# Performance work log

Measured on AMD Instinct MI355X. Metric: run time of the kernel, lower is better.

The kernel has to match this reference:

```python
import jax, jax.numpy as jnp
import numpy as np

HIDDEN = 256
N_HEADS = 4
HEAD_DIM = HIDDEN // N_HEADS
SCALE = float(np.sqrt(HEAD_DIM))


def setup_inputs() -> dict:
    key = jax.random.key(0)
    ks = jax.random.split(key, 10)
    B, NQ, NKV = 2, 4096, 4096
    s = 1.0 / np.sqrt(HIDDEN)
    inp = {
        "query": jax.random.normal(ks[0], (B, NQ, HIDDEN), dtype=jnp.float32),
        "key_value": jax.random.normal(ks[1], (B, NKV, HIDDEN), dtype=jnp.float32),
        "kv_mask": jnp.ones((B, NKV), dtype=jnp.int32),
        "Wq": jax.random.uniform(ks[2], (HIDDEN, HIDDEN), jnp.float32, -s, s),
        "bq": jnp.zeros((HIDDEN,), jnp.float32),
        "Wk": jax.random.uniform(ks[3], (HIDDEN, HIDDEN), jnp.float32, -s, s),
        "bk": jnp.zeros((HIDDEN,), jnp.float32),
        "Wv": jax.random.uniform(ks[4], (HIDDEN, HIDDEN), jnp.float32, -s, s),
        "bv": jnp.zeros((HIDDEN,), jnp.float32),
        "Wo": jax.random.uniform(ks[5], (HIDDEN, HIDDEN), jnp.float32, -s, s),
        "bo": jnp.zeros((HIDDEN,), jnp.float32),
    }
    return inp


def reference(query, key_value, kv_mask, Wq, bq, Wk, bk, Wv, bv, Wo, bo):
    B, NQ, D = query.shape
    NKV = key_value.shape[1]
    # projections; reshape to (B, H, S, Dh)
    q = (query @ Wq + bq).reshape(B, NQ, N_HEADS, HEAD_DIM).transpose(0, 2, 1, 3)
    k = (key_value @ Wk + bk).reshape(B, NKV, N_HEADS, HEAD_DIM).transpose(0, 2, 1, 3)
    v = (key_value @ Wv + bv).reshape(B, NKV, N_HEADS, HEAD_DIM).transpose(0, 2, 1, 3)
    # scores: (B, H, NQ, NKV)
    attn = jnp.einsum("bhqd,bhkd->bhqk", q, k) / SCALE
    mask = (kv_mask != 0)[:, None, None, :]  # (B,1,1,NKV)
    attn = jnp.where(mask, attn, -jnp.inf)
    attn = jax.nn.softmax(attn, axis=-1)
    # dropout is identity in eval mode (reference is deterministic)
    out = jnp.einsum("bhqk,bhkd->bhqd", attn, v)
    out = out.transpose(0, 2, 1, 3).reshape(B, NQ, D)
    return out @ Wo + bo
```

## Files before the change

kernel.cpp:

```cpp
#include <hip/hip_runtime.h>
#include <hip/hip_bf16.h>
#include <math.h>

#define HID   256
#define NHEADS  4
#define HDIM   64
#define SEQ  4096
#define BATCH   2
#define MTOK (BATCH * SEQ)
#define LOG2E 1.44269504088896340736f
#define MFIX  8.0f

typedef short bf16x8 __attribute__((ext_vector_type(8)));
typedef float f32x4  __attribute__((ext_vector_type(4)));

__device__ __forceinline__ unsigned short f2b(float f) {
  union { float f; unsigned u; } v; v.f = f;
  return (unsigned short)((v.u + 0x7FFFu + ((v.u >> 16) & 1u)) >> 16);
}
__device__ __forceinline__ unsigned pkb(float a, float b) {
  __hip_bfloat162 h = __float22bfloat162_rn(make_float2(a, b));
  union { __hip_bfloat162 h; unsigned u; } v; v.h = h;
  return v.u;
}
__device__ __forceinline__ float exp2_(float x) {
#if __has_builtin(__builtin_amdgcn_exp2f)
  return __builtin_amdgcn_exp2f(x);
#else
  return exp2f(x);
#endif
}

__global__ __launch_bounds__(256)
void cast_wt(const float* __restrict__ W0, const float* __restrict__ W1,
             const float* __restrict__ W2, const float* __restrict__ W3,
             unsigned short* __restrict__ Wt) {
  __shared__ float t[64][65];
  const float* Ws[4] = {W0, W1, W2, W3};
  const float scl[4] = {0.125f * LOG2E, 1.f, 1.f, 1.f};
  const int wsel = blockIdx.y;
  const float* W = Ws[wsel];
  const float s = scl[wsel];
  unsigned short* O = Wt + (size_t)wsel * HID * HID;
  const int kt = (blockIdx.x & 3) * 64, nt = (blockIdx.x >> 2) * 64;
  const int tid = threadIdx.x;
#pragma unroll
  for (int p = 0; p < 4; ++p) {
    int i = p * 256 + tid;
    int r = i >> 4, c4 = (i & 15) * 4;
    *(float4*)&t[r][c4] = *(const float4*)&W[(size_t)(kt + r) * HID + nt + c4];
  }
  __syncthreads();
#pragma unroll
  for (int p = 0; p < 4; ++p) {
    int i = p * 256 + tid;
    int rn = i >> 4, ck = (i & 15) * 4;
    ushort4 o;
    o.x = f2b(t[ck + 0][rn] * s);
    o.y = f2b(t[ck + 1][rn] * s);
    o.z = f2b(t[ck + 2][rn] * s);
    o.w = f2b(t[ck + 3][rn] * s);
    *(ushort4*)&O[(size_t)(nt + rn) * HID + kt + ck] = o;
  }
}

__global__ __launch_bounds__(256)
void gemm_qkv(const float* __restrict__ query, const float* __restrict__ keyv,
              const unsigned short* __restrict__ wts,
              const float* __restrict__ bq, const float* __restrict__ bk,
              const float* __restrict__ bv,
              unsigned short* qp, unsigned short* kp, unsigned short* vtp) {
  __shared__ __align__(16) unsigned short As[2][64][136];
  __shared__ __align__(16) unsigned short Bs[64][136];
  float (*L)[68] = (float (*)[68])&Bs[0][0];

  const int tid = threadIdx.x;
  const int w = tid >> 6, lane = tid & 63, lq = lane & 15, quad = lane >> 4;
  const int wm = w & 1, wn = w >> 1;
  const int z = blockIdx.y;
  const int m0 = blockIdx.x * 64;

  const float* A = (z == 0) ? query : keyv;
  const unsigned short* Bt = wts + (size_t)z * HID * HID;
  const float* bias = (z == 0) ? bq : ((z == 1) ? bk : bv);
  const float bscale = (z == 0) ? 0.125f * LOG2E : 1.0f;

#pragma unroll
  for (int p = 0; p < 16; ++p) {
    int i = p * 256 + tid;
    int r = i >> 6, c4 = (i & 63) * 4;
    float4 f4 = *(const float4*)&A[(size_t)(m0 + r) * HID + c4];
    unsigned lo = pkb(f4.x, f4.y), hi = pkb(f4.z, f4.w);
    *(uint2*)&As[c4 >> 7][r][c4 & 127] = make_uint2(lo, hi);
  }
  __syncthreads();

  for (int n = 0; n < 4; ++n) {
    const int n0 = n * 64;
    f32x4 acc[2][2];
#pragma unroll
    for (int i = 0; i < 2; ++i)
#pragma unroll
      for (int j = 0; j < 2; ++j) acc[i][j] = (f32x4){0.f, 0.f, 0.f, 0.f};

#pragma unroll
    for (int kt = 0; kt < 2; ++kt) {
#pragma unroll
      for (int p = 0; p < 4; ++p) {
        int i = p * 256 + tid;
        int r = i >> 4, c8 = (i & 15) * 8;
        *(uint4*)&Bs[r][c8] =
            *(const uint4*)&Bt[(size_t)(n0 + r) * HID + kt * 128 + c8];
      }
      __syncthreads();
#pragma unroll
      for (int ks = 0; ks < 4; ++ks) {
        bf16x8 a0 = *(const bf16x8*)&As[kt][wm * 32 + lq][ks * 32 + quad * 8];
        bf16x8 a1 = *(const bf16x8*)&As[kt][wm * 32 + 16 + lq][ks * 32 + quad * 8];
        bf16x8 b0 = *(const bf16x8*)&Bs[wn * 32 + lq][ks * 32 + quad * 8];
        bf16x8 b1 = *(const bf16x8*)&Bs[wn * 32 + 16 + lq][ks * 32 + quad * 8];
        acc[0][0] = __builtin_amdgcn_mfma_f32_16x16x32_bf16(a0, b0, acc[0][0], 0, 0, 0);
        acc[0][1] = __builtin_amdgcn_mfma_f32_16x16x32_bf16(a0, b1, acc[0][1], 0, 0, 0);
        acc[1][0] = __builtin_amdgcn_mfma_f32_16x16x32_bf16(a1, b0, acc[1][0], 0, 0, 0);
        acc[1][1] = __builtin_amdgcn_mfma_f32_16x16x32_bf16(a1, b1, acc[1][1], 0, 0, 0);
      }
      __syncthreads();
    }

#pragma unroll
    for (int ni = 0; ni < 2; ++ni) {
      const float bv = bias[n0 + wn * 32 + ni * 16 + lq] * bscale;
#pragma unroll
      for (int mi = 0; mi < 2; ++mi)
#pragma unroll
        for (int r = 0; r < 4; ++r)
          L[wm * 32 + mi * 16 + quad * 4 + r][wn * 32 + ni * 16 + lq] =
              acc[mi][ni][r] + bv;
    }
    __syncthreads();

    if (z == 2) {
      const int nn = tid >> 2, mb4 = (tid & 3) * 16;
      __align__(16) unsigned short tmp[16];
#pragma unroll
      for (int j = 0; j < 16; ++j) {
        int p = mb4 + j;
        int k = ((p & 3) << 4) + (p >> 2);
        tmp[j] = f2b(L[k][nn]);
      }
      *(uint4*)&vtp[(size_t)(n0 + nn) * MTOK + m0 + mb4]     = *(uint4*)&tmp[0];
      *(uint4*)&vtp[(size_t)(n0 + nn) * MTOK + m0 + mb4 + 8] = *(uint4*)&tmp[8];
    } else {
      unsigned short* Y = (z == 0) ? qp : kp;
      const int r = tid >> 2, cb = (tid & 3) * 16;
      __align__(16) unsigned short tmp[16];
#pragma unroll
      for (int j = 0; j < 4; ++j) {
        float4 v4 = *(const float4*)&L[r][cb + j * 4];
        *(uint2*)&tmp[j * 4] = make_uint2(pkb(v4.x, v4.y), pkb(v4.z, v4.w));
      }
      *(uint4*)&Y[(size_t)(m0 + r) * HID + n0 + cb]     = *(uint4*)&tmp[0];
      *(uint4*)&Y[(size_t)(m0 + r) * HID + n0 + cb + 8] = *(uint4*)&tmp[8];
    }
    __syncthreads();
  }
}

__global__ __launch_bounds__(256)
void gemm_out(const unsigned short* __restrict__ ao,
              const unsigned short* __restrict__ wot,
              const float* __restrict__ bo, float* __restrict__ out) {
  __shared__ __align__(16) unsigned short As[64][136];
  __shared__ __align__(16) unsigned short Bs[64][136];
  float (*L)[68] = (float (*)[68])&As[0][0];

  const int tid = threadIdx.x;
  const int w = tid >> 6, lane = tid & 63, lq = lane & 15, quad = lane >> 4;
  const int wm = w & 1, wn = w >> 1;
  const int m0 = blockIdx.y * 64, n0 = blockIdx.x * 64;

  f32x4 acc[2][2];
#pragma unroll
  for (int i = 0; i < 2; ++i)
#pragma unroll
    for (int j = 0; j < 2; ++j) acc[i][j] = (f32x4){0.f, 0.f, 0.f, 0.f};

#pragma unroll
  for (int kt = 0; kt < 2; ++kt) {
    const int k0 = kt * 128;
#pragma unroll
    for (int p = 0; p < 4; ++p) {
      int i = p * 256 + tid;
      int r = i >> 4, c8 = (i & 15) * 8;
      *(uint4*)&As[r][c8] = *(const uint4*)&ao[(size_t)(m0 + r) * HID + k0 + c8];
      *(uint4*)&Bs[r][c8] = *(const uint4*)&wot[(size_t)(n0 + r) * HID + k0 + c8];
    }
    __syncthreads();
#pragma unroll
    for (int ks = 0; ks < 4; ++ks) {
      bf16x8 a0 = *(const bf16x8*)&As[wm * 32 + lq][ks * 32 + quad * 8];
      bf16x8 a1 = *(const bf16x8*)&As[wm * 32 + 16 + lq][ks * 32 + quad * 8];
      bf16x8 b0 = *(const bf16x8*)&Bs[wn * 32 + lq][ks * 32 + quad * 8];
      bf16x8 b1 = *(const bf16x8*)&Bs[wn * 32 + 16 + lq][ks * 32 + quad * 8];
      acc[0][0] = __builtin_amdgcn_mfma_f32_16x16x32_bf16(a0, b0, acc[0][0], 0, 0, 0);
      acc[0][1] = __builtin_amdgcn_mfma_f32_16x16x32_bf16(a0, b1, acc[0][1], 0, 0, 0);
      acc[1][0] = __builtin_amdgcn_mfma_f32_16x16x32_bf16(a1, b0, acc[1][0], 0, 0, 0);
      acc[1][1] = __builtin_amdgcn_mfma_f32_16x16x32_bf16(a1, b1, acc[1][1], 0, 0, 0);
    }
    __syncthreads();
  }

#pragma unroll
  for (int ni = 0; ni < 2; ++ni) {
    const float bv = bo[n0 + wn * 32 + ni * 16 + lq];
#pragma unroll
    for (int mi = 0; mi < 2; ++mi)
#pragma unroll
      for (int r = 0; r < 4; ++r)
        L[wm * 32 + mi * 16 + quad * 4 + r][wn * 32 + ni * 16 + lq] =
            acc[mi][ni][r] + bv;
  }
  __syncthreads();

  const int r = tid >> 2, cb = (tid & 3) * 16;
#pragma unroll
  for (int j = 0; j < 4; ++j) {
    float4 v4 = *(const float4*)&L[r][cb + j * 4];
    *(float4*)&out[(size_t)(m0 + r) * HID + n0 + cb + j * 4] = v4;
  }
}

__global__ __launch_bounds__(512, 1)
void flash_attn_mfma(const unsigned short* __restrict__ Qp,
                     const unsigned short* __restrict__ Kp,
                     const unsigned short* __restrict__ Vtp,
                     const int* __restrict__ mask,
                     unsigned short* __restrict__ Ao) {
  __shared__ __align__(16) unsigned short Ks[2][128][72];
  __shared__ __align__(16) unsigned short Vt[2][64][136];
  __shared__ __align__(16) unsigned short Ps[8][32][72];
  __shared__ float mb[2][128];

  float (*Ored)[32][68] = (float (*)[32][68])&Ps[0][0][0];
  float* Lred = (float*)((char*)&Ps[0][0][0] + sizeof(float) * 4 * 32 * 68);

  const int tid = threadIdx.x;
  const int w = tid >> 6, lane = tid & 63, lq = lane & 15, quad = lane >> 4;
  const int qg = w >> 1, kg = w & 1;
  const int bh = blockIdx.x;
  const int b = bh >> 2, h = bh & 3;
  const int q0 = blockIdx.y * 128;
  const int qbase = b * SEQ + q0, kvbase = b * SEQ, coff = h * HDIM;

  const int rk0 = tid >> 3,          ck0 = (tid & 7) * 8;
  const int rk1 = (512 + tid) >> 3,  ck1 = ((512 + tid) & 7) * 8;
  const int rv0 = tid >> 4,          cv0 = (tid & 15) * 8;
  const int rv1 = (512 + tid) >> 4,  cv1 = ((512 + tid) & 15) * 8;

  bf16x8 qf[2][2];
#pragma unroll
  for (int m = 0; m < 2; ++m) {
    const unsigned short* qr =
        &Qp[(size_t)(qbase + qg * 32 + m * 16 + lq) * HID + coff + quad * 8];
    qf[m][0] = *(const bf16x8*)&qr[0];
    qf[m][1] = *(const bf16x8*)&qr[32];
  }

  const short oneb = (short)0x3F80;
  const bf16x8 ones = {oneb, oneb, oneb, oneb, oneb, oneb, oneb, oneb};

  f32x4 o[2][4], ls2[2];
#pragma unroll
  for (int m = 0; m < 2; ++m) {
    ls2[m] = (f32x4){0.f, 0.f, 0.f, 0.f};
#pragma unroll
    for (int dc = 0; dc < 4; ++dc) o[m][dc] = (f32x4){0.f, 0.f, 0.f, 0.f};
  }

  {
    *(uint4*)&Ks[0][rk0][ck0] =
        *(const uint4*)&Kp[(size_t)(kvbase + rk0) * HID + coff + ck0];
    *(uint4*)&Ks[0][rk1][ck1] =
        *(const uint4*)&Kp[(size_t)(kvbase + rk1) * HID + coff + ck1];
    *(uint4*)&Vt[0][rv0][cv0] =
        *(const uint4*)&Vtp[(size_t)(coff + rv0) * MTOK + kvbase + cv0];
    *(uint4*)&Vt[0][rv1][cv1] =
        *(const uint4*)&Vtp[(size_t)(coff + rv1) * MTOK + kvbase + cv1];
    if (tid < 128) mb[0][tid] = mask[kvbase + tid] ? -MFIX : -1e30f;
  }
  __syncthreads();

  const int NT = SEQ / 128;
  for (int t = 0; t < NT; ++t) {
    const int cur = t & 1, nxt = cur ^ 1;
    const bool pf = (t + 1 < NT);

    uint4 kA, kB, vA, vB;
    float mbr = 0.f;
    if (pf) {
      const int k0n = (t + 1) * 128;
      kA = *(const uint4*)&Kp[(size_t)(kvbase + k0n + rk0) * HID + coff + ck0];
      kB = *(const uint4*)&Kp[(size_t)(kvbase + k0n + rk1) * HID + coff + ck1];
      vA = *(const uint4*)&Vtp[(size_t)(coff + rv0) * MTOK + kvbase + k0n + cv0];
      vB = *(const uint4*)&Vtp[(size_t)(coff + rv1) * MTOK + kvbase + k0n + cv1];
      if (tid < 128) mbr = mask[kvbase + k0n + tid] ? -MFIX : -1e30f;
    }

    f32x4 sc[2][4];
#pragma unroll
    for (int m = 0; m < 2; ++m)
#pragma unroll
      for (int c = 0; c < 4; ++c) sc[m][c] = (f32x4){0.f, 0.f, 0.f, 0.f};
#pragma unroll
    for (int c = 0; c < 4; ++c) {
      bf16x8 kb0 = *(const bf16x8*)&Ks[cur][kg * 64 + c * 16 + lq][quad * 8];
      bf16x8 kb1 = *(const bf16x8*)&Ks[cur][kg * 64 + c * 16 + lq][32 + quad * 8];
      sc[0][c] = __builtin_amdgcn_mfma_f32_16x16x32_bf16(qf[0][0], kb0, sc[0][c], 0, 0, 0);
      sc[0][c] = __builtin_amdgcn_mfma_f32_16x16x32_bf16(qf[0][1], kb1, sc[0][c], 0, 0, 0);
      sc[1][c] = __builtin_amdgcn_mfma_f32_16x16x32_bf16(qf[1][0], kb0, sc[1][c], 0, 0, 0);
      sc[1][c] = __builtin_amdgcn_mfma_f32_16x16x32_bf16(qf[1][1], kb1, sc[1][c], 0, 0, 0);
    }
    float mbias[4];
#pragma unroll
    for (int c = 0; c < 4; ++c) mbias[c] = mb[cur][kg * 64 + c * 16 + lq];

#pragma unroll
    for (int m = 0; m < 2; ++m) {
#pragma unroll
      for (int r = 0; r < 4; ++r) {
        const int row = m * 16 + quad * 4 + r;
        unsigned a0 = pkb(exp2_(sc[m][0][r] + mbias[0]),
                          exp2_(sc[m][1][r] + mbias[1]));
        unsigned a1 = pkb(exp2_(sc[m][2][r] + mbias[2]),
                          exp2_(sc[m][3][r] + mbias[3]));
        *(uint2*)&Ps[w][row][lq * 4] = make_uint2(a0, a1);
      }
    }

#pragma unroll
    for (int i = 0; i < 2; ++i) {
      bf16x8 pa0 = *(const bf16x8*)&Ps[w][lq][i * 32 + quad * 8];
      bf16x8 pa1 = *(const bf16x8*)&Ps[w][16 + lq][i * 32 + quad * 8];
      ls2[0] = __builtin_amdgcn_mfma_f32_16x16x32_bf16(pa0, ones, ls2[0], 0, 0, 0);
      ls2[1] = __builtin_amdgcn_mfma_f32_16x16x32_bf16(pa1, ones, ls2[1], 0, 0, 0);
#pragma unroll
      for (int dc = 0; dc < 4; ++dc) {
        bf16x8 vb =
            *(const bf16x8*)&Vt[cur][dc * 16 + lq][kg * 64 + i * 32 + quad * 8];
        o[0][dc] = __builtin_amdgcn_mfma_f32_16x16x32_bf16(pa0, vb, o[0][dc], 0, 0, 0);
        o[1][dc] = __builtin_amdgcn_mfma_f32_16x16x32_bf16(pa1, vb, o[1][dc], 0, 0, 0);
      }
    }

    if (pf) {
      *(uint4*)&Ks[nxt][rk0][ck0] = kA;
      *(uint4*)&Ks[nxt][rk1][ck1] = kB;
      *(uint4*)&Vt[nxt][rv0][cv0] = vA;
      *(uint4*)&Vt[nxt][rv1][cv1] = vB;
      if (tid < 128) mb[nxt][tid] = mbr;
    }
    __syncthreads();
  }

  if (kg == 1) {
#pragma unroll
    for (int m = 0; m < 2; ++m) {
#pragma unroll
      for (int r = 0; r < 4; ++r) {
        const int row = m * 16 + quad * 4 + r;
        if (lq == 0) Lred[qg * 32 + row] = ls2[m][r];
#pragma unroll
        for (int dc = 0; dc < 4; ++dc)
          Ored[qg][row][dc * 16 + lq] = o[m][dc][r];
      }
    }
  }
  __syncthreads();
  if (kg == 0) {
#pragma unroll
    for (int m = 0; m < 2; ++m) {
#pragma unroll
      for (int r = 0; r < 4; ++r) {
        const int row = m * 16 + quad * 4 + r;
        const float l = ls2[m][r] + Lred[qg * 32 + row];
        const float inv = 1.f / l;
        const size_t grow = (size_t)(qbase + qg * 32 + row);
#pragma unroll
        for (int dc = 0; dc < 4; ++dc) {
          const float val = (o[m][dc][r] + Ored[qg][row][dc * 16 + lq]) * inv;
          Ao[grow * HID + coff + dc * 16 + lq] = f2b(val);
        }
      }
    }
  }
}

extern "C" void kernel_launch(void* const* d_in, const int* in_sizes, int n_in,
                              void* d_out, int out_size, void* d_ws, size_t ws_size,
                              hipStream_t stream) {
  const float* query = (const float*)d_in[0];
  const float* keyv  = (const float*)d_in[1];
  const int*   mask  = (const int*)d_in[2];
  const float* Wq = (const float*)d_in[3];
  const float* bq = (const float*)d_in[4];
  const float* Wk = (const float*)d_in[5];
  const float* bk = (const float*)d_in[6];
  const float* Wv = (const float*)d_in[7];
  const float* bv = (const float*)d_in[8];
  const float* Wo = (const float*)d_in[9];
  const float* bo = (const float*)d_in[10];
  float* out = (float*)d_out;

  unsigned short* wts = (unsigned short*)d_ws;
  unsigned short* qp  = wts + (size_t)4 * HID * HID;
  unsigned short* kp  = qp  + (size_t)MTOK * HID;
  unsigned short* vtp = kp  + (size_t)MTOK * HID;
  unsigned short* ao  = vtp + (size_t)MTOK * HID;

  const unsigned short* wo_t = wts + 3 * HID * HID;

  dim3 blk(256);
  hipLaunchKernelGGL(cast_wt, dim3(16, 4), blk, 0, stream, Wq, Wk, Wv, Wo, wts);

  dim3 qkvgrid(MTOK / 64, 3);
  hipLaunchKernelGGL(gemm_qkv, qkvgrid, blk, 0, stream,
                     query, keyv, wts, bq, bk, bv, qp, kp, vtp);

  dim3 fgrid(BATCH * NHEADS, SEQ / 128);
  hipLaunchKernelGGL(flash_attn_mfma, fgrid, dim3(512), 0, stream,
                     qp, kp, vtp, mask, ao);

  dim3 ogrid(HID / 64, MTOK / 64);
  hipLaunchKernelGGL(gemm_out, ogrid, blk, 0, stream, ao, wo_t, bo, out);
}
```

Before: 159.5 us.

## Fuse weight transpose-cast into projection GEMMs and drop cast kernel

Removes the separate weight cast/transpose kernel. The QKV and output GEMMs now read fp32 weights directly, scale and convert them to bf16, and scatter them transposed into shared memory. The output GEMM is restructured so each block holds a 64-row A tile and loops over all four N tiles, matching the QKV kernel. This saves one kernel launch and a workspace round trip. In exchange, every block redoes the weight conversion with scalar 2-byte transposed LDS stores that may bank-conflict, and the output GEMM grid shrinks fourfold.

```diff
diff --git a/kernel.cpp b/kernel.cpp
--- a/kernel.cpp
+++ b/kernel.cpp
@@ -32,41 +32,9 @@
 }
 
 __global__ __launch_bounds__(256)
-void cast_wt(const float* __restrict__ W0, const float* __restrict__ W1,
-             const float* __restrict__ W2, const float* __restrict__ W3,
-             unsigned short* __restrict__ Wt) {
-  __shared__ float t[64][65];
-  const float* Ws[4] = {W0, W1, W2, W3};
-  const float scl[4] = {0.125f * LOG2E, 1.f, 1.f, 1.f};
-  const int wsel = blockIdx.y;
-  const float* W = Ws[wsel];
-  const float s = scl[wsel];
-  unsigned short* O = Wt + (size_t)wsel * HID * HID;
-  const int kt = (blockIdx.x & 3) * 64, nt = (blockIdx.x >> 2) * 64;
-  const int tid = threadIdx.x;
-#pragma unroll
-  for (int p = 0; p < 4; ++p) {
-    int i = p * 256 + tid;
-    int r = i >> 4, c4 = (i & 15) * 4;
-    *(float4*)&t[r][c4] = *(const float4*)&W[(size_t)(kt + r) * HID + nt + c4];
-  }
-  __syncthreads();
-#pragma unroll
-  for (int p = 0; p < 4; ++p) {
-    int i = p * 256 + tid;
-    int rn = i >> 4, ck = (i & 15) * 4;
-    ushort4 o;
-    o.x = f2b(t[ck + 0][rn] * s);
-    o.y = f2b(t[ck + 1][rn] * s);
-    o.z = f2b(t[ck + 2][rn] * s);
-    o.w = f2b(t[ck + 3][rn] * s);
-    *(ushort4*)&O[(size_t)(nt + rn) * HID + kt + ck] = o;
-  }
-}
-
-__global__ __launch_bounds__(256)
 void gemm_qkv(const float* __restrict__ query, const float* __restrict__ keyv,
-              const unsigned short* __restrict__ wts,
+              const float* __restrict__ Wq, const float* __restrict__ Wk,
+              const float* __restrict__ Wv,
               const float* __restrict__ bq, const float* __restrict__ bk,
               const float* __restrict__ bv,
               unsigned short* qp, unsigned short* kp, unsigned short* vtp) {
@@ -81,7 +49,7 @@
   const int m0 = blockIdx.x * 64;
 
   const float* A = (z == 0) ? query : keyv;
-  const unsigned short* Bt = wts + (size_t)z * HID * HID;
+  const float* Wz = (z == 0) ? Wq : ((z == 1) ? Wk : Wv);
   const float* bias = (z == 0) ? bq : ((z == 1) ? bk : bv);
   const float bscale = (z == 0) ? 0.125f * LOG2E : 1.0f;
 
@@ -106,11 +74,15 @@
 #pragma unroll
     for (int kt = 0; kt < 2; ++kt) {
 #pragma unroll
-      for (int p = 0; p < 4; ++p) {
+      for (int p = 0; p < 8; ++p) {
         int i = p * 256 + tid;
-        int r = i >> 4, c8 = (i & 15) * 8;
-        *(uint4*)&Bs[r][c8] =
-            *(const uint4*)&Bt[(size_t)(n0 + r) * HID + kt * 128 + c8];
+        int kr = i >> 4;
+        int ng = (i & 15) * 4;
+        float4 wv4 = *(const float4*)&Wz[(size_t)(kt * 128 + kr) * HID + n0 + ng];
+        Bs[ng + 0][kr] = f2b(wv4.x * bscale);
+        Bs[ng + 1][kr] = f2b(wv4.y * bscale);
+        Bs[ng + 2][kr] = f2b(wv4.z * bscale);
+        Bs[ng + 3][kr] = f2b(wv4.w * bscale);
       }
       __syncthreads();
 #pragma unroll
@@ -168,65 +140,81 @@
 
 __global__ __launch_bounds__(256)
 void gemm_out(const unsigned short* __restrict__ ao,
-              const unsigned short* __restrict__ wot,
+              const float* __restrict__ Wo,
               const float* __restrict__ bo, float* __restrict__ out) {
-  __shared__ __align__(16) unsigned short As[64][136];
+  __shared__ __align__(16) unsigned short As[2][64][136];
   __shared__ __align__(16) unsigned short Bs[64][136];
-  float (*L)[68] = (float (*)[68])&As[0][0];
+  float (*L)[68] = (float (*)[68])&Bs[0][0];
 
   const int tid = threadIdx.x;
   const int w = tid >> 6, lane = tid & 63, lq = lane & 15, quad = lane >> 4;
   const int wm = w & 1, wn = w >> 1;
-  const int m0 = blockIdx.y * 64, n0 = blockIdx.x * 64;
-
-  f32x4 acc[2][2];
-#pragma unroll
-  for (int i = 0; i < 2; ++i)
-#pragma unroll
-    for (int j = 0; j < 2; ++j) acc[i][j] = (f32x4){0.f, 0.f, 0.f, 0.f};
-
-#pragma unroll
-  for (int kt = 0; kt < 2; ++kt) {
-    const int k0 = kt * 128;
-#pragma unroll
-    for (int p = 0; p < 4; ++p) {
-      int i = p * 256 + tid;
-      int r = i >> 4, c8 = (i & 15) * 8;
-      *(uint4*)&As[r][c8] = *(const uint4*)&ao[(size_t)(m0 + r) * HID + k0 + c8];
-      *(uint4*)&Bs[r][c8] = *(const uint4*)&wot[(size_t)(n0 + r) * HID + k0 + c8];
+  const int m0 = blockIdx.x * 64;
+
+#pragma unroll
+  for (int p = 0; p < 8; ++p) {
+    int i = p * 256 + tid;
+    int r = i >> 5, c8 = (i & 31) * 8;
+    *(uint4*)&As[c8 >> 7][r][c8 & 127] =
+        *(const uint4*)&ao[(size_t)(m0 + r) * HID + c8];
+  }
+  __syncthreads();
+
+  for (int n = 0; n < 4; ++n) {
+    const int n0 = n * 64;
+    f32x4 acc[2][2];
+#pragma unroll
+    for (int i = 0; i < 2; ++i)
+#pragma unroll
+      for (int j = 0; j < 2; ++j) acc[i][j] = (f32x4){0.f, 0.f, 0.f, 0.f};
+
+#pragma unroll
+    for (int kt = 0; kt < 2; ++kt) {
+#pragma unroll
+      for (int p = 0; p < 8; ++p) {
+        int i = p * 256 + tid;
+        int kr = i >> 4;
+        int ng = (i & 15) * 4;
+        float4 wv4 = *(const float4*)&Wo[(size_t)(kt * 128 + kr) * HID + n0 + ng];
+        Bs[ng + 0][kr] = f2b(wv4.x);
+        Bs[ng + 1][kr] = f2b(wv4.y);
+        Bs[ng + 2][kr] = f2b(wv4.z);
+        Bs[ng + 3][kr] = f2b(wv4.w);
+      }
+      __syncthreads();
+#pragma unroll
+      for (int ks = 0; ks < 4; ++ks) {
+        bf16x8 a0 = *(const bf16x8*)&As[kt][wm * 32 + lq][ks * 32 + quad * 8];
+        bf16x8 a1 = *(const bf16x8*)&As[kt][wm * 32 + 16 + lq][ks * 32 + quad * 8];
+        bf16x8 b0 = *(const bf16x8*)&Bs[wn * 32 + lq][ks * 32 + quad * 8];
+        bf16x8 b1 = *(const bf16x8*)&Bs[wn * 32 + 16 + lq][ks * 32 + quad * 8];
+        acc[0][0] = __builtin_amdgcn_mfma_f32_16x16x32_bf16(a0, b0, acc[0][0], 0, 0, 0);
+        acc[0][1] = __builtin_amdgcn_mfma_f32_16x16x32_bf16(a0, b1, acc[0][1], 0, 0, 0);
+        acc[1][0] = __builtin_amdgcn_mfma_f32_16x16x32_bf16(a1, b0, acc[1][0], 0, 0, 0);
+        acc[1][1] = __builtin_amdgcn_mfma_f32_16x16x32_bf16(a1, b1, acc[1][1], 0, 0, 0);
+      }
+      __syncthreads();
+    }
+
+#pragma unroll
+    for (int ni = 0; ni < 2; ++ni) {
+      const float bv = bo[n0 + wn * 32 + ni * 16 + lq];
+#pragma unroll
+      for (int mi = 0; mi < 2; ++mi)
+#pragma unroll
+        for (int r = 0; r < 4; ++r)
+          L[wm * 32 + mi * 16 + quad * 4 + r][wn * 32 + ni * 16 + lq] =
+              acc[mi][ni][r] + bv;
     }
     __syncthreads();
-#pragma unroll
-    for (int ks = 0; ks < 4; ++ks) {
-      bf16x8 a0 = *(const bf16x8*)&As[wm * 32 + lq][ks * 32 + quad * 8];
-      bf16x8 a1 = *(const bf16x8*)&As[wm * 32 + 16 + lq][ks * 32 + quad * 8];
-      bf16x8 b0 = *(const bf16x8*)&Bs[wn * 32 + lq][ks * 32 + quad * 8];
-      bf16x8 b1 = *(const bf16x8*)&Bs[wn * 32 + 16 + lq][ks * 32 + quad * 8];
-      acc[0][0] = __builtin_amdgcn_mfma_f32_16x16x32_bf16(a0, b0, acc[0][0], 0, 0, 0);
-      acc[0][1] = __builtin_amdgcn_mfma_f32_16x16x32_bf16(a0, b1, acc[0][1], 0, 0, 0);
-      acc[1][0] = __builtin_amdgcn_mfma_f32_16x16x32_bf16(a1, b0, acc[1][0], 0, 0, 0);
-      acc[1][1] = __builtin_amdgcn_mfma_f32_16x16x32_bf16(a1, b1, acc[1][1], 0, 0, 0);
+
+    const int r = tid >> 2, cb = (tid & 3) * 16;
+#pragma unroll
+    for (int j = 0; j < 4; ++j) {
+      float4 v4 = *(const float4*)&L[r][cb + j * 4];
+      *(float4*)&out[(size_t)(m0 + r) * HID + n0 + cb + j * 4] = v4;
     }
     __syncthreads();
-  }
-
-#pragma unroll
-  for (int ni = 0; ni < 2; ++ni) {
-    const float bv = bo[n0 + wn * 32 + ni * 16 + lq];
-#pragma unroll
-    for (int mi = 0; mi < 2; ++mi)
-#pragma unroll
-      for (int r = 0; r < 4; ++r)
-        L[wm * 32 + mi * 16 + quad * 4 + r][wn * 32 + ni * 16 + lq] =
-            acc[mi][ni][r] + bv;
-  }
-  __syncthreads();
-
-  const int r = tid >> 2, cb = (tid & 3) * 16;
-#pragma unroll
-  for (int j = 0; j < 4; ++j) {
-    float4 v4 = *(const float4*)&L[r][cb + j * 4];
-    *(float4*)&out[(size_t)(m0 + r) * HID + n0 + cb + j * 4] = v4;
   }
 }
 
@@ -411,25 +399,20 @@
   const float* bo = (const float*)d_in[10];
   float* out = (float*)d_out;
 
-  unsigned short* wts = (unsigned short*)d_ws;
-  unsigned short* qp  = wts + (size_t)4 * HID * HID;
+  unsigned short* qp  = (unsigned short*)d_ws;
   unsigned short* kp  = qp  + (size_t)MTOK * HID;
   unsigned short* vtp = kp  + (size_t)MTOK * HID;
   unsigned short* ao  = vtp + (size_t)MTOK * HID;
 
-  const unsigned short* wo_t = wts + 3 * HID * HID;
-
   dim3 blk(256);
-  hipLaunchKernelGGL(cast_wt, dim3(16, 4), blk, 0, stream, Wq, Wk, Wv, Wo, wts);
-
   dim3 qkvgrid(MTOK / 64, 3);
   hipLaunchKernelGGL(gemm_qkv, qkvgrid, blk, 0, stream,
-                     query, keyv, wts, bq, bk, bv, qp, kp, vtp);
+                     query, keyv, Wq, Wk, Wv, bq, bk, bv, qp, kp, vtp);
 
   dim3 fgrid(BATCH * NHEADS, SEQ / 128);
   hipLaunchKernelGGL(flash_attn_mfma, fgrid, dim3(512), 0, stream,
                      qp, kp, vtp, mask, ao);
 
-  dim3 ogrid(HID / 64, MTOK / 64);
-  hipLaunchKernelGGL(gemm_out, ogrid, blk, 0, stream, ao, wo_t, bo, out);
-}
+  dim3 ogrid(MTOK / 64);
+  hipLaunchKernelGGL(gemm_out, ogrid, blk, 0, stream, ao, Wo, bo, out);
+}
```

Result: slower. 183.0 us (+14.7%).

## Repartition attention waves into 2 query groups by 4 key groups

Applied to the files above, without the earlier changes.

Changes the flash-attention wave split from 4 query groups × 2 key groups to 2 query groups × 4 key groups. Each wave now owns 64 query rows and 32 keys per tile, so every K and V fragment read from LDS feeds four MFMA row tiles instead of two. The V-transpose permutation in the projection kernel and the P staging layout change to match the new 32-key slice. The final cross-wave reduction becomes a two-stage tree that reuses the K/V/mask shared buffers. This trades higher per-wave register use for the accumulators and Q fragments, plus an extra sync stage in the epilogue, against less LDS traffic per MFMA.

```diff
diff --git a/kernel.cpp b/kernel.cpp
--- a/kernel.cpp
+++ b/kernel.cpp
@@ -145,7 +145,8 @@
 #pragma unroll
       for (int j = 0; j < 16; ++j) {
         int p = mb4 + j;
-        int k = ((p & 3) << 4) + (p >> 2);
+        int p32 = p & 31, g = p >> 5;
+        int k = g * 32 + ((p32 & 1) << 4) + (p32 >> 1);
         tmp[j] = f2b(L[k][nn]);
       }
       *(uint4*)&vtp[(size_t)(n0 + nn) * MTOK + m0 + mb4]     = *(uint4*)&tmp[0];
@@ -238,15 +239,17 @@
                      unsigned short* __restrict__ Ao) {
   __shared__ __align__(16) unsigned short Ks[2][128][72];
   __shared__ __align__(16) unsigned short Vt[2][64][136];
-  __shared__ __align__(16) unsigned short Ps[8][32][72];
+  __shared__ __align__(16) unsigned short Ps[8][64][40];
   __shared__ float mb[2][128];
 
-  float (*Ored)[32][68] = (float (*)[32][68])&Ps[0][0][0];
-  float* Lred = (float*)((char*)&Ps[0][0][0] + sizeof(float) * 4 * 32 * 68);
+  float (*OredA)[64][68] = (float (*)[64][68])&Ks[0][0][0];
+  float (*OredB)[64][68] = (float (*)[64][68])&Vt[0][0][0];
+  float* LredA = (float*)&mb[0][0];
+  float* LredB = (float*)&mb[1][0];
 
   const int tid = threadIdx.x;
   const int w = tid >> 6, lane = tid & 63, lq = lane & 15, quad = lane >> 4;
-  const int qg = w >> 1, kg = w & 1;
+  const int qg = w >> 2, kg = w & 3;
   const int bh = blockIdx.x;
   const int b = bh >> 2, h = bh & 3;
   const int q0 = blockIdx.y * 128;
@@ -257,11 +260,11 @@
   const int rv0 = tid >> 4,          cv0 = (tid & 15) * 8;
   const int rv1 = (512 + tid) >> 4,  cv1 = ((512 + tid) & 15) * 8;
 
-  bf16x8 qf[2][2];
-#pragma unroll
-  for (int m = 0; m < 2; ++m) {
+  bf16x8 qf[4][2];
+#pragma unroll
+  for (int m = 0; m < 4; ++m) {
     const unsigned short* qr =
-        &Qp[(size_t)(qbase + qg * 32 + m * 16 + lq) * HID + coff + quad * 8];
+        &Qp[(size_t)(qbase + qg * 64 + m * 16 + lq) * HID + coff + quad * 8];
     qf[m][0] = *(const bf16x8*)&qr[0];
     qf[m][1] = *(const bf16x8*)&qr[32];
   }
@@ -269,9 +272,9 @@
   const short oneb = (short)0x3F80;
   const bf16x8 ones = {oneb, oneb, oneb, oneb, oneb, oneb, oneb, oneb};
 
-  f32x4 o[2][4], ls2[2];
-#pragma unroll
-  for (int m = 0; m < 2; ++m) {
+  f32x4 o[4][4], ls2[4];
+#pragma unroll
+  for (int m = 0; m < 4; ++m) {
     ls2[m] = (f32x4){0.f, 0.f, 0.f, 0.f};
 #pragma unroll
     for (int dc = 0; dc < 4; ++dc) o[m][dc] = (f32x4){0.f, 0.f, 0.f, 0.f};
@@ -306,49 +309,44 @@
       if (tid < 128) mbr = mask[kvbase + k0n + tid] ? -MFIX : -1e30f;
     }
 
-    f32x4 sc[2][4];
-#pragma unroll
-    for (int m = 0; m < 2; ++m)
-#pragma unroll
-      for (int c = 0; c < 4; ++c) sc[m][c] = (f32x4){0.f, 0.f, 0.f, 0.f};
-#pragma unroll
-    for (int c = 0; c < 4; ++c) {
-      bf16x8 kb0 = *(const bf16x8*)&Ks[cur][kg * 64 + c * 16 + lq][quad * 8];
-      bf16x8 kb1 = *(const bf16x8*)&Ks[cur][kg * 64 + c * 16 + lq][32 + quad * 8];
-      sc[0][c] = __builtin_amdgcn_mfma_f32_16x16x32_bf16(qf[0][0], kb0, sc[0][c], 0, 0, 0);
-      sc[0][c] = __builtin_amdgcn_mfma_f32_16x16x32_bf16(qf[0][1], kb1, sc[0][c], 0, 0, 0);
-      sc[1][c] = __builtin_amdgcn_mfma_f32_16x16x32_bf16(qf[1][0], kb0, sc[1][c], 0, 0, 0);
-      sc[1][c] = __builtin_amdgcn_mfma_f32_16x16x32_bf16(qf[1][1], kb1, sc[1][c], 0, 0, 0);
-    }
-    float mbias[4];
-#pragma unroll
-    for (int c = 0; c < 4; ++c) mbias[c] = mb[cur][kg * 64 + c * 16 + lq];
-
-#pragma unroll
-    for (int m = 0; m < 2; ++m) {
+    f32x4 sc[4][2];
+#pragma unroll
+    for (int m = 0; m < 4; ++m)
+#pragma unroll
+      for (int c = 0; c < 2; ++c) sc[m][c] = (f32x4){0.f, 0.f, 0.f, 0.f};
+#pragma unroll
+    for (int c = 0; c < 2; ++c) {
+      bf16x8 kb0 = *(const bf16x8*)&Ks[cur][kg * 32 + c * 16 + lq][quad * 8];
+      bf16x8 kb1 = *(const bf16x8*)&Ks[cur][kg * 32 + c * 16 + lq][32 + quad * 8];
+#pragma unroll
+      for (int m = 0; m < 4; ++m) {
+        sc[m][c] = __builtin_amdgcn_mfma_f32_16x16x32_bf16(qf[m][0], kb0, sc[m][c], 0, 0, 0);
+        sc[m][c] = __builtin_amdgcn_mfma_f32_16x16x32_bf16(qf[m][1], kb1, sc[m][c], 0, 0, 0);
+      }
+    }
+    float mbias[2];
+#pragma unroll
+    for (int c = 0; c < 2; ++c) mbias[c] = mb[cur][kg * 32 + c * 16 + lq];
+
+#pragma unroll
+    for (int m = 0; m < 4; ++m) {
 #pragma unroll
       for (int r = 0; r < 4; ++r) {
         const int row = m * 16 + quad * 4 + r;
-        unsigned a0 = pkb(exp2_(sc[m][0][r] + mbias[0]),
-                          exp2_(sc[m][1][r] + mbias[1]));
-        unsigned a1 = pkb(exp2_(sc[m][2][r] + mbias[2]),
-                          exp2_(sc[m][3][r] + mbias[3]));
-        *(uint2*)&Ps[w][row][lq * 4] = make_uint2(a0, a1);
-      }
-    }
-
-#pragma unroll
-    for (int i = 0; i < 2; ++i) {
-      bf16x8 pa0 = *(const bf16x8*)&Ps[w][lq][i * 32 + quad * 8];
-      bf16x8 pa1 = *(const bf16x8*)&Ps[w][16 + lq][i * 32 + quad * 8];
-      ls2[0] = __builtin_amdgcn_mfma_f32_16x16x32_bf16(pa0, ones, ls2[0], 0, 0, 0);
-      ls2[1] = __builtin_amdgcn_mfma_f32_16x16x32_bf16(pa1, ones, ls2[1], 0, 0, 0);
+        *(unsigned*)&Ps[w][row][lq * 2] =
+            pkb(exp2_(sc[m][0][r] + mbias[0]), exp2_(sc[m][1][r] + mbias[1]));
+      }
+    }
+
+#pragma unroll
+    for (int m = 0; m < 4; ++m) {
+      bf16x8 pa = *(const bf16x8*)&Ps[w][m * 16 + lq][quad * 8];
+      ls2[m] = __builtin_amdgcn_mfma_f32_16x16x32_bf16(pa, ones, ls2[m], 0, 0, 0);
 #pragma unroll
       for (int dc = 0; dc < 4; ++dc) {
         bf16x8 vb =
-            *(const bf16x8*)&Vt[cur][dc * 16 + lq][kg * 64 + i * 32 + quad * 8];
-        o[0][dc] = __builtin_amdgcn_mfma_f32_16x16x32_bf16(pa0, vb, o[0][dc], 0, 0, 0);
-        o[1][dc] = __builtin_amdgcn_mfma_f32_16x16x32_bf16(pa1, vb, o[1][dc], 0, 0, 0);
+            *(const bf16x8*)&Vt[cur][dc * 16 + lq][kg * 32 + quad * 8];
+        o[m][dc] = __builtin_amdgcn_mfma_f32_16x16x32_bf16(pa, vb, o[m][dc], 0, 0, 0);
       }
     }
 
@@ -362,32 +360,64 @@
     __syncthreads();
   }
 
-  if (kg == 1) {
-#pragma unroll
-    for (int m = 0; m < 2; ++m) {
+  if (kg >= 2) {
+    float (*Ob)[64][68] = (kg == 2) ? OredA : OredB;
+    float* Lb = (kg == 2) ? LredA : LredB;
+#pragma unroll
+    for (int m = 0; m < 4; ++m) {
 #pragma unroll
       for (int r = 0; r < 4; ++r) {
         const int row = m * 16 + quad * 4 + r;
-        if (lq == 0) Lred[qg * 32 + row] = ls2[m][r];
+        if (lq == 0) Lb[qg * 64 + row] = ls2[m][r];
 #pragma unroll
         for (int dc = 0; dc < 4; ++dc)
-          Ored[qg][row][dc * 16 + lq] = o[m][dc][r];
-      }
-    }
-  }
-  __syncthreads();
-  if (kg == 0) {
-#pragma unroll
-    for (int m = 0; m < 2; ++m) {
+          Ob[qg][row][dc * 16 + lq] = o[m][dc][r];
+      }
+    }
+  }
+  __syncthreads();
+  if (kg < 2) {
+    float (*Ob)[64][68] = (kg == 0) ? OredA : OredB;
+    float* Lb = (kg == 0) ? LredA : LredB;
+#pragma unroll
+    for (int m = 0; m < 4; ++m) {
 #pragma unroll
       for (int r = 0; r < 4; ++r) {
         const int row = m * 16 + quad * 4 + r;
-        const float l = ls2[m][r] + Lred[qg * 32 + row];
+        ls2[m][r] += Lb[qg * 64 + row];
+#pragma unroll
+        for (int dc = 0; dc < 4; ++dc)
+          o[m][dc][r] += Ob[qg][row][dc * 16 + lq];
+      }
+    }
+  }
+  __syncthreads();
+  if (kg == 1) {
+#pragma unroll
+    for (int m = 0; m < 4; ++m) {
+#pragma unroll
+      for (int r = 0; r < 4; ++r) {
+        const int row = m * 16 + quad * 4 + r;
+        if (lq == 0) LredA[qg * 64 + row] = ls2[m][r];
+#pragma unroll
+        for (int dc = 0; dc < 4; ++dc)
+          OredA[qg][row][dc * 16 + lq] = o[m][dc][r];
+      }
+    }
+  }
+  __syncthreads();
+  if (kg == 0) {
+#pragma unroll
+    for (int m = 0; m < 4; ++m) {
+#pragma unroll
+      for (int r = 0; r < 4; ++r) {
+        const int row = m * 16 + quad * 4 + r;
+        const float l = ls2[m][r] + LredA[qg * 64 + row];
         const float inv = 1.f / l;
-        const size_t grow = (size_t)(qbase + qg * 32 + row);
+        const size_t grow = (size_t)(qbase + qg * 64 + row);
 #pragma unroll
         for (int dc = 0; dc < 4; ++dc) {
-          const float val = (o[m][dc][r] + Ored[qg][row][dc * 16 + lq]) * inv;
+          const float val = (o[m][dc][r] + OredA[qg][row][dc * 16 + lq]) * inv;
           Ao[grow * HID + coff + dc * 16 + lq] = f2b(val);
         }
       }
```

Result: no change. 158.6 us (-0.6%).
